# Kernel tuning notes

Hardware: AMD Instinct MI355X
Metric: run time of the kernel (lower is better)

## Reference

```python
import jax, jax.numpy as jnp
import numpy as np

EPS = 1e-5

def _bn(x, gamma, beta):
    # x: [B, N, C]; training-mode BatchNorm1d over (B, N)
    mu = jnp.mean(x, axis=(0, 1))
    var = jnp.var(x, axis=(0, 1))
    return (x - mu) * jax.lax.rsqrt(var + EPS) * gamma + beta


def setup_inputs() -> dict:
    key = jax.random.key(0)
    ks = jax.random.split(key, 32)
    B, N = 16, 8192
    enc_dim, mem_dim = 1024, 1024
    feat_dim = enc_dim + mem_dim  # 2048
    n_points = 2048
    s = 0.02
    d = {
        'partial': jax.random.normal(ks[0], (B, N, 3), jnp.float32),
        # first_conv: Conv1d(3,128,1) + BN(128) + ReLU + Conv1d(128,256,1)
        'W1': jax.random.normal(ks[1], (128, 3), jnp.float32) * s,
        'b1': jnp.zeros((128,), jnp.float32),
        'g1': jnp.ones((128,), jnp.float32),
        'be1': jnp.zeros((128,), jnp.float32),
        'W2': jax.random.normal(ks[2], (256, 128), jnp.float32) * s,
        'b2': jnp.zeros((256,), jnp.float32),
        # second_conv: Conv1d(512,512,1) + BN(512) + ReLU + Conv1d(512,enc_dim,1)
        'W3': jax.random.normal(ks[3], (512, 512), jnp.float32) * s,
        'b3': jnp.zeros((512,), jnp.float32),
        'g2': jnp.ones((512,), jnp.float32),
        'be2': jnp.zeros((512,), jnp.float32),
        'W4': jax.random.normal(ks[4], (enc_dim, 512), jnp.float32) * s,
        'b4': jnp.zeros((enc_dim,), jnp.float32),
        # MemoryModule gates: Linear(enc_dim, mem_dim) x4 + memory param
        'Wf': jax.random.normal(ks[5], (mem_dim, enc_dim), jnp.float32) * s,
        'bf': jnp.zeros((mem_dim,), jnp.float32),
        'Wi': jax.random.normal(ks[6], (mem_dim, enc_dim), jnp.float32) * s,
        'bi': jnp.zeros((mem_dim,), jnp.float32),
        'Wo': jax.random.normal(ks[7], (mem_dim, enc_dim), jnp.float32) * s,
        'bo': jnp.zeros((mem_dim,), jnp.float32),
        'Wc': jax.random.normal(ks[8], (mem_dim, enc_dim), jnp.float32) * s,
        'bc': jnp.zeros((mem_dim,), jnp.float32),
        'mem': jax.random.normal(ks[9], (1, mem_dim), jnp.float32),
        # Decoder MLP: feat_dim->2048->2048->2048->3*n_points
        'D1w': jax.random.normal(ks[10], (2048, feat_dim), jnp.float32) * s,
        'D1b': jnp.zeros((2048,), jnp.float32),
        'D2w': jax.random.normal(ks[11], (2048, 2048), jnp.float32) * s,
        'D2b': jnp.zeros((2048,), jnp.float32),
        'D3w': jax.random.normal(ks[12], (2048, 2048), jnp.float32) * s,
        'D3b': jnp.zeros((2048,), jnp.float32),
        'D4w': jax.random.normal(ks[13], (3 * n_points, 2048), jnp.float32) * s,
        'D4b': jnp.zeros((3 * n_points,), jnp.float32),
    }
    return d


def reference(partial, W1, b1, g1, be1, W2, b2, W3, b3, g2, be2, W4, b4,
              Wf, bf, Wi, bi, Wo, bo, Wc, bc, mem,
              D1w, D1b, D2w, D2b, D3w, D3b, D4w, D4b):
    B, N, _ = partial.shape
    # --- Encoder first_conv (pointwise convs == per-point linear) ---
    f = jnp.einsum('bnc,dc->bnd', partial, W1) + b1          # [B,N,128]
    f = jax.nn.relu(_bn(f, g1, be1))
    f = jnp.einsum('bnc,dc->bnd', f, W2) + b2                # [B,N,256]
    fg = jnp.max(f, axis=1, keepdims=True)                   # [B,1,256]
    f = jnp.concatenate([jnp.broadcast_to(fg, (B, N, 256)), f], axis=-1)  # [B,N,512]
    # --- second_conv ---
    f = jnp.einsum('bnc,dc->bnd', f, W3) + b3                # [B,N,512]
    f = jax.nn.relu(_bn(f, g2, be2))
    f = jnp.einsum('bnc,dc->bnd', f, W4) + b4                # [B,N,enc_dim]
    feat_global = jnp.max(f, axis=1)                         # [B,enc_dim]
    # --- MemoryModule (flag=False: memory not updated) ---
    fgate = jax.nn.sigmoid(feat_global @ Wf.T + bf)
    igate = jax.nn.sigmoid(feat_global @ Wi.T + bi)
    ogate = jax.nn.sigmoid(feat_global @ Wo.T + bo)
    cand = jnp.tanh(feat_global @ Wc.T + bc)
    mem_b = jnp.broadcast_to(mem, fgate.shape)
    h = ogate * jnp.tanh(fgate * mem_b + igate * cand)       # [B,mem_dim]
    feat = jnp.concatenate([feat_global, h], axis=1)         # [B,feat_dim]
    # --- Decoder MLP ---
    z = jax.nn.relu(feat @ D1w.T + D1b)
    z = jax.nn.relu(z @ D2w.T + D2b)
    z = jax.nn.relu(z @ D3w.T + D3b)
    z = z @ D4w.T + D4b                                      # [B, 3*n_points]
    return z.reshape(B, -1, 3)
```

## Files before the change

### kernel.cpp

```cpp
#include <hip/hip_runtime.h>
#include <hip/hip_bf16.h>

typedef __bf16 v8bf __attribute__((ext_vector_type(8)));
typedef float  v4f  __attribute__((ext_vector_type(4)));

#define NPTS (16*8192)
#define RPB  8192

#define GLOAD_LDS16(g, l) __builtin_amdgcn_global_load_lds( \
    (const __attribute__((address_space(1))) void*)(g), \
    (__attribute__((address_space(3))) void*)(l), 16, 0, 0)

__device__ __forceinline__ unsigned fenc(float x){
    unsigned u = __float_as_uint(x);
    return (u & 0x80000000u) ? ~u : (u | 0x80000000u);
}
__device__ __forceinline__ float fdec(unsigned u){
    return __uint_as_float((u & 0x80000000u) ? (u ^ 0x80000000u) : ~u);
}

__device__ __forceinline__ v8bf bn_relu8(v8bf v, float4 s0, float4 s1, float4 h0, float4 h1){
    v8bf r;
    r[0] = (__bf16)fmaxf(fmaf((float)v[0], s0.x, h0.x), 0.f);
    r[1] = (__bf16)fmaxf(fmaf((float)v[1], s0.y, h0.y), 0.f);
    r[2] = (__bf16)fmaxf(fmaf((float)v[2], s0.z, h0.z), 0.f);
    r[3] = (__bf16)fmaxf(fmaf((float)v[3], s0.w, h0.w), 0.f);
    r[4] = (__bf16)fmaxf(fmaf((float)v[4], s1.x, h1.x), 0.f);
    r[5] = (__bf16)fmaxf(fmaf((float)v[5], s1.y, h1.y), 0.f);
    r[6] = (__bf16)fmaxf(fmaf((float)v[6], s1.z, h1.z), 0.f);
    r[7] = (__bf16)fmaxf(fmaf((float)v[7], s1.w, h1.w), 0.f);
    return r;
}

__global__ __launch_bounds__(256) void stats1_k(const float* __restrict__ P,
        const float* __restrict__ W1, const float* __restrict__ b1,
        float* __restrict__ gsum, float* __restrict__ gsumsq)
{
    int tid = threadIdx.x;
    int c = tid & 127, half = tid >> 7;
    float w0 = W1[c*3+0], w1 = W1[c*3+1], w2 = W1[c*3+2], bb = b1[c];
    float s = 0.f, s2 = 0.f;
    int base = blockIdx.x * 512 + half;
    for (int i = 0; i < 256; ++i) {
        int p = base + i*2;
        float x = P[p*3+0], y = P[p*3+1], z = P[p*3+2];
        float v = fmaf(w0,x, fmaf(w1,y, fmaf(w2,z, bb)));
        s += v; s2 = fmaf(v,v,s2);
    }
    __shared__ float ls[256], lq[256];
    ls[tid] = s; lq[tid] = s2;
    __syncthreads();
    if (half == 0) {
        atomicAdd(&gsum[c],   s  + ls[tid+128]);
        atomicAdd(&gsumsq[c], s2 + lq[tid+128]);
    }
}

__global__ void finalize_k(const float* __restrict__ gsum, const float* __restrict__ gsumsq,
        const float* __restrict__ gamma, const float* __restrict__ beta,
        float* __restrict__ scale, float* __restrict__ shift, int C, float invn)
{
    int c = blockIdx.x*blockDim.x + threadIdx.x;
    if (c >= C) return;
    float m   = gsum[c]*invn;
    float var = fmaxf(gsumsq[c]*invn - m*m, 0.f);
    float rs  = rsqrtf(var + 1e-5f);
    float sc  = gamma[c]*rs;
    scale[c] = sc;
    shift[c] = beta[c] - m*sc;
}

__global__ void cvt3_k(const float* __restrict__ W2, const float* __restrict__ W3,
                       const float* __restrict__ W4,
                       __bf16* __restrict__ W2b, __bf16* __restrict__ W3bb,
                       __bf16* __restrict__ W4b)
{
    int i = blockIdx.x*256 + threadIdx.x;
    if (i < 32768) {
        W2b[i] = (__bf16)W2[i];
    } else if (i < 32768 + 131072) {
        int k = i - 32768;
        int r = k >> 8, c = k & 255;
        W3bb[k] = (__bf16)W3[(size_t)r*512 + 256 + c];
    } else if (i < 32768 + 131072 + 524288) {
        int k = i - 163840;
        W4b[k] = (__bf16)W4[k];
    }
}

template<bool STORE, bool DOMAX, bool STATS, int BNMODE, int LOGNB>
__global__ __launch_bounds__(256, 2) void gemm_k(
        const __bf16* __restrict__ A, const __bf16* __restrict__ Bw,
        int K, int Nw,
        const float* __restrict__ bias, int bias_bstride,
        __bf16* __restrict__ Cout, unsigned* __restrict__ maxenc,
        float* __restrict__ gsum, float* __restrict__ gsq,
        const float* __restrict__ scA, const float* __restrict__ shA,
        const float* __restrict__ P3, const float* __restrict__ W1,
        const float* __restrict__ b1)
{
    __shared__ __bf16 As[128*64];
    __shared__ __bf16 Bs[256*64];
    __shared__ float lstat[2][2][256];

    const int tid  = threadIdx.x;
    const int lane = tid & 63;
    const int wave = tid >> 6;
    const int wr = wave >> 1, wc = wave & 1;
    const int nwg   = (int)gridDim.x;
    const int chunk = nwg >> 3;
    const int bi    = (int)blockIdx.x;
    const int li    = (bi & 7) * chunk + (bi >> 3);
    const int m0    = (li >> LOGNB) * 128;
    const int n0    = (li & ((1 << LOGNB) - 1)) * 256;
    const int srow = tid >> 3, sslot = tid & 7;
    const int lrow  = lane >> 3;
    const int swz   = ((lane & 7) ^ lrow) * 8;

    v4f acc[4][8];
    #pragma unroll
    for (int i=0;i<4;i++)
      #pragma unroll
      for (int j=0;j<8;j++) acc[i][j] = (v4f)(0.0f);

    v8bf ra[4];
    auto loadA_pre = [&](int kb){
        int kk = kb + sslot*8;
        float4 s0 = *(const float4*)(scA + kk);
        float4 s1 = *(const float4*)(scA + kk + 4);
        float4 h0 = *(const float4*)(shA + kk);
        float4 h1 = *(const float4*)(shA + kk + 4);
        if constexpr (BNMODE == 1) {
            #pragma unroll
            for (int i=0;i<4;i++){
                int r = i*32 + srow;
                v8bf v = *(const v8bf*)(A + (size_t)(m0+r)*K + kb + sslot*8);
                ra[i] = bn_relu8(v, s0, s1, h0, h1);
            }
        } else if constexpr (BNMODE == 2) {
            float wv0[8], wv1[8], wv2[8], bb[8];
            #pragma unroll
            for (int e=0;e<8;e++){
                wv0[e] = W1[(kk+e)*3+0];
                wv1[e] = W1[(kk+e)*3+1];
                wv2[e] = W1[(kk+e)*3+2];
                bb[e]  = b1[kk+e];
            }
            float sarr[8] = {s0.x,s0.y,s0.z,s0.w,s1.x,s1.y,s1.z,s1.w};
            float harr[8] = {h0.x,h0.y,h0.z,h0.w,h1.x,h1.y,h1.z,h1.w};
            #pragma unroll
            for (int i=0;i<4;i++){
                int r = i*32 + srow;
                const float* pp = P3 + (size_t)(m0+r)*3;
                float x = pp[0], y = pp[1], z = pp[2];
                v8bf v;
                #pragma unroll
                for (int e=0;e<8;e++){
                    float t = fmaf(wv0[e],x, fmaf(wv1[e],y, fmaf(wv2[e],z, bb[e])));
                    t = fmaxf(fmaf(t, sarr[e], harr[e]), 0.f);
                    v[e] = (__bf16)t;
                }
                ra[i] = v;
            }
        }
    };
    auto stageB = [&](int kb){
        #pragma unroll
        for (int j=0;j<8;j++){
            int r0 = (wave*8 + j)*8;
            GLOAD_LDS16(Bw + (size_t)(n0 + r0 + lrow)*K + kb + swz, &Bs[r0*64]);
        }
    };
    auto stageA = [&](int kb){
        #pragma unroll
        for (int j=0;j<4;j++){
            int r0 = (wave*4 + j)*8;
            GLOAD_LDS16(A + (size_t)(m0 + r0 + lrow)*K + kb + swz, &As[r0*64]);
        }
    };

    if constexpr (BNMODE != 0) loadA_pre(0);

    for (int k0 = 0; k0 < K; k0 += 64) {
        __syncthreads();
        stageB(k0);
        if constexpr (BNMODE != 0) {
            #pragma unroll
            for (int i=0;i<4;i++){
                int r = i*32 + srow;
                *(v8bf*)(&As[r*64 + ((sslot ^ (r & 7))<<3)]) = ra[i];
            }
        } else {
            stageA(k0);
        }
        __syncthreads();
        if constexpr (BNMODE != 0) { if (k0 + 64 < K) loadA_pre(k0 + 64); }
        #pragma unroll
        for (int kk = 0; kk < 2; ++kk) {
            v8bf af[4], bfr[8];
            #pragma unroll
            for (int i=0;i<4;i++){
                int arow = wr*64 + i*16 + (lane & 15);
                int sg = kk*4 + (lane >> 4);
                af[i] = *(const v8bf*)(&As[arow*64 + ((sg ^ (arow & 7))<<3)]);
            }
            #pragma unroll
            for (int j=0;j<8;j++){
                int brow = wc*128 + j*16 + (lane & 15);
                int sg = kk*4 + (lane >> 4);
                bfr[j] = *(const v8bf*)(&Bs[brow*64 + ((sg ^ (brow & 7))<<3)]);
            }
            #pragma unroll
            for (int i=0;i<4;i++)
              #pragma unroll
              for (int j=0;j<8;j++)
                acc[i][j] = __builtin_amdgcn_mfma_f32_16x16x32_bf16(af[i], bfr[j], acc[i][j], 0,0,0);
        }
    }

    const int b = m0 / RPB;
    const float* brow_ = bias + (size_t)b * bias_bstride;
    float colmax[8], csum[8], csq[8];
    #pragma unroll
    for (int j=0;j<8;j++){ colmax[j] = -3.402823466e38f; csum[j]=0.f; csq[j]=0.f; }

    #pragma unroll
    for (int i=0;i<4;i++){
        int rbase = m0 + wr*64 + i*16 + ((lane>>4)<<2);
        #pragma unroll
        for (int j=0;j<8;j++){
            int col = n0 + wc*128 + j*16 + (lane & 15);
            float bv = brow_[col];
            #pragma unroll
            for (int q=0;q<4;q++){
                float v = acc[i][j][q] + bv;
                if constexpr (STORE) Cout[(size_t)(rbase+q)*Nw + col] = (__bf16)v;
                if constexpr (DOMAX) colmax[j] = fmaxf(colmax[j], v);
                if constexpr (STATS) { csum[j] += v; csq[j] = fmaf(v,v,csq[j]); }
            }
        }
    }
    if constexpr (DOMAX) {
        #pragma unroll
        for (int j=0;j<8;j++){
            float v = colmax[j];
            v = fmaxf(v, __shfl_xor(v, 16));
            v = fmaxf(v, __shfl_xor(v, 32));
            if (lane < 16) {
                int col = n0 + wc*128 + j*16 + lane;
                atomicMax(&maxenc[(size_t)b*Nw + col], fenc(v));
            }
        }
    }
    if constexpr (STATS) {
        #pragma unroll
        for (int j=0;j<8;j++){
            float s = csum[j], q = csq[j];
            s += __shfl_xor(s, 16); s += __shfl_xor(s, 32);
            q += __shfl_xor(q, 16); q += __shfl_xor(q, 32);
            if (lane < 16) {
                int c = wc*128 + j*16 + lane;
                lstat[0][wr][c] = s;
                lstat[1][wr][c] = q;
            }
        }
        __syncthreads();
        if (tid < 256) {
            float s = lstat[0][0][tid] + lstat[0][1][tid];
            float q = lstat[1][0][tid] + lstat[1][1][tid];
            atomicAdd(&gsum[n0 + tid], s);
            atomicAdd(&gsq [n0 + tid], q);
        }
    }
}

__global__ __launch_bounds__(256) void bias3_k(const unsigned* __restrict__ fge,
        const float* __restrict__ W3, const float* __restrict__ b3,
        float* __restrict__ bias3)
{
    int b = blockIdx.x, tid = threadIdx.x;
    __shared__ float fg[256];
    fg[tid] = fdec(fge[b*256 + tid]);
    __syncthreads();
    for (int d = tid; d < 512; d += 256) {
        const float* wrow = W3 + (size_t)d*512;
        float s = b3[d];
        for (int c = 0; c < 256; c += 4) {
            s = fmaf(fg[c+0], wrow[c+0], s);
            s = fmaf(fg[c+1], wrow[c+1], s);
            s = fmaf(fg[c+2], wrow[c+2], s);
            s = fmaf(fg[c+3], wrow[c+3], s);
        }
        bias3[b*512 + d] = s;
    }
}

__global__ __launch_bounds__(256) void gates2_k(const unsigned* __restrict__ enc,
        const float* __restrict__ Wf, const float* __restrict__ bfv,
        const float* __restrict__ Wi, const float* __restrict__ biv,
        const float* __restrict__ Wo, const float* __restrict__ bov,
        const float* __restrict__ Wc, const float* __restrict__ bcv,
        const float* __restrict__ memv, float* __restrict__ feat)
{
    int tid = threadIdx.x;
    int b = tid & 15;
    int j = blockIdx.x*16 + (tid >> 4);
    const unsigned* xe = enc + (size_t)b*1024;
    const float* rf = Wf + (size_t)j*1024;
    const float* ri = Wi + (size_t)j*1024;
    const float* ro = Wo + (size_t)j*1024;
    const float* rc = Wc + (size_t)j*1024;
    float sf = bfv[j], si = biv[j], so = bov[j], scn = bcv[j];
    for (int c = 0; c < 1024; c += 4) {
        uint4 u = *(const uint4*)(xe + c);
        float4 xv = { fdec(u.x), fdec(u.y), fdec(u.z), fdec(u.w) };
        float4 a  = *(const float4*)(rf + c);
        sf = fmaf(xv.x,a.x, fmaf(xv.y,a.y, fmaf(xv.z,a.z, fmaf(xv.w,a.w, sf))));
        float4 bq = *(const float4*)(ri + c);
        si = fmaf(xv.x,bq.x, fmaf(xv.y,bq.y, fmaf(xv.z,bq.z, fmaf(xv.w,bq.w, si))));
        float4 cq = *(const float4*)(ro + c);
        so = fmaf(xv.x,cq.x, fmaf(xv.y,cq.y, fmaf(xv.z,cq.z, fmaf(xv.w,cq.w, so))));
        float4 dq = *(const float4*)(rc + c);
        scn= fmaf(xv.x,dq.x, fmaf(xv.y,dq.y, fmaf(xv.z,dq.z, fmaf(xv.w,dq.w, scn))));
    }
    float fg = 1.f/(1.f + expf(-sf));
    float ig = 1.f/(1.f + expf(-si));
    float og = 1.f/(1.f + expf(-so));
    float cd = tanhf(scn);
    float h  = og * tanhf(fmaf(fg, memv[j], ig*cd));
    feat[(size_t)b*2048 + j]        = fdec(enc[(size_t)b*1024 + j]);
    feat[(size_t)b*2048 + 1024 + j] = h;
}

template<bool RELU>
__global__ __launch_bounds__(256) void dec2_k(const float* __restrict__ in,
        const float* __restrict__ W, const float* __restrict__ bias,
        float* __restrict__ out, int N)
{
    __shared__ float xin[16*2048];
    int tid = threadIdx.x;
    int lane = tid & 63, wv = tid >> 6;
    #pragma unroll
    for (int j = 0; j < 32; ++j) {
        int blk = wv*32 + j;
        GLOAD_LDS16(in + blk*256 + lane*4, &xin[blk*256]);
    }
    __syncthreads();
    #pragma unroll
    for (int c = 0; c < 2; ++c) {
        int col = blockIdx.x*8 + wv*2 + c;
        const float* wrow = W + (size_t)col*2048;
        float s[16];
        #pragma unroll
        for (int b=0;b<16;b++) s[b]=0.f;
        #pragma unroll
        for (int it = 0; it < 8; ++it) {
            int k = it*256 + lane*4;
            float4 w4 = *(const float4*)(wrow + k);
            #pragma unroll
            for (int b=0;b<16;b++){
                const float* xb = &xin[b*2048 + k];
                s[b] = fmaf(w4.x, xb[0], fmaf(w4.y, xb[1], fmaf(w4.z, xb[2], fmaf(w4.w, xb[3], s[b]))));
            }
        }
        #pragma unroll
        for (int off=32; off; off>>=1){
            #pragma unroll
            for (int b=0;b<16;b++) s[b] += __shfl_xor(s[b], off);
        }
        if (lane == 0) {
            float bv = bias[col];
            #pragma unroll
            for (int b=0;b<16;b++){
                float v = s[b] + bv;
                if (RELU) v = fmaxf(v, 0.f);
                out[(size_t)b*N + col] = v;
            }
        }
    }
}

extern "C" void kernel_launch(void* const* d_in, const int* in_sizes, int n_in,
                              void* d_out, int out_size, void* d_ws, size_t ws_size,
                              hipStream_t stream)
{
    (void)in_sizes; (void)n_in; (void)out_size; (void)ws_size;
    const float* partial = (const float*)d_in[0];
    const float* W1 = (const float*)d_in[1];
    const float* b1 = (const float*)d_in[2];
    const float* g1 = (const float*)d_in[3];
    const float* be1= (const float*)d_in[4];
    const float* W2 = (const float*)d_in[5];
    const float* b2 = (const float*)d_in[6];
    const float* W3 = (const float*)d_in[7];
    const float* b3 = (const float*)d_in[8];
    const float* g2 = (const float*)d_in[9];
    const float* be2= (const float*)d_in[10];
    const float* W4 = (const float*)d_in[11];
    const float* b4 = (const float*)d_in[12];
    const float* Wf = (const float*)d_in[13];
    const float* bfv= (const float*)d_in[14];
    const float* Wi = (const float*)d_in[15];
    const float* biv= (const float*)d_in[16];
    const float* Wo = (const float*)d_in[17];
    const float* bov= (const float*)d_in[18];
    const float* Wc = (const float*)d_in[19];
    const float* bcv= (const float*)d_in[20];
    const float* memv=(const float*)d_in[21];
    const float* D1w= (const float*)d_in[22];
    const float* D1b= (const float*)d_in[23];
    const float* D2w= (const float*)d_in[24];
    const float* D2b= (const float*)d_in[25];
    const float* D3w= (const float*)d_in[26];
    const float* D3b= (const float*)d_in[27];
    const float* D4w= (const float*)d_in[28];
    const float* D4b= (const float*)d_in[29];

    char* w = (char*)d_ws;
    size_t off = 0;
    auto alloc = [&](size_t bytes) -> void* {
        void* p = w + off; off += (bytes + 255) & ~(size_t)255; return p;
    };
    __bf16* f2   = (__bf16*)alloc((size_t)NPTS*256*2);
    __bf16* y3   = (__bf16*)alloc((size_t)NPTS*512*2);
    __bf16* W2b  = (__bf16*)alloc(256*128*2);
    __bf16* W3bb = (__bf16*)alloc(512*256*2);
    __bf16* W4b  = (__bf16*)alloc(1024*512*2);
    char* accbase = (char*)(w + off);
    float* gsum1    = (float*)alloc(128*4);
    float* gsumsq1  = (float*)alloc(128*4);
    float* gsum3    = (float*)alloc(512*4);
    float* gsumsq3  = (float*)alloc(512*4);
    unsigned* fg_enc    = (unsigned*)alloc(16*256*4);
    unsigned* featg_enc = (unsigned*)alloc(16*1024*4);
    size_t accbytes = (size_t)((w + off) - accbase);
    float* scale1 = (float*)alloc(128*4);
    float* shift1 = (float*)alloc(128*4);
    float* scale3 = (float*)alloc(512*4);
    float* shift3 = (float*)alloc(512*4);
    float* bias3  = (float*)alloc(16*512*4);
    float* feat   = (float*)alloc(16*2048*4);
    float* z1     = (float*)alloc(16*2048*4);
    float* z2     = (float*)alloc(16*2048*4);
    float* z3     = (float*)alloc(16*2048*4);

    hipMemsetAsync(accbase, 0, accbytes, stream);

    cvt3_k<<<dim3(2688), 256, 0, stream>>>(W2, W3, W4, W2b, W3bb, W4b);

    stats1_k<<<dim3(256), 256, 0, stream>>>(partial, W1, b1, gsum1, gsumsq1);
    finalize_k<<<dim3(1), 128, 0, stream>>>(gsum1, gsumsq1, g1, be1, scale1, shift1, 128, 1.f/NPTS);

    gemm_k<true,true,false,2,0><<<dim3(1024), 256, 0, stream>>>(
        nullptr, W2b, 128, 256, b2, 0, f2, fg_enc, nullptr, nullptr,
        scale1, shift1, partial, W1, b1);

    bias3_k<<<dim3(16), 256, 0, stream>>>(fg_enc, W3, b3, bias3);

    gemm_k<true,false,true,0,1><<<dim3(2048), 256, 0, stream>>>(
        f2, W3bb, 256, 512, bias3, 512, y3, nullptr, gsum3, gsumsq3,
        nullptr, nullptr, nullptr, nullptr, nullptr);

    finalize_k<<<dim3(2), 256, 0, stream>>>(gsum3, gsumsq3, g2, be2, scale3, shift3, 512, 1.f/NPTS);

    gemm_k<false,true,false,1,2><<<dim3(4096), 256, 0, stream>>>(
        y3, W4b, 512, 1024, b4, 0, nullptr, featg_enc, nullptr, nullptr,
        scale3, shift3, nullptr, nullptr, nullptr);

    gates2_k<<<dim3(64), 256, 0, stream>>>(featg_enc, Wf,bfv, Wi,biv, Wo,bov, Wc,bcv, memv, feat);

    dec2_k<true ><<<dim3(256), 256, 0, stream>>>(feat, D1w, D1b, z1, 2048);
    dec2_k<true ><<<dim3(256), 256, 0, stream>>>(z1,   D2w, D2b, z2, 2048);
    dec2_k<true ><<<dim3(256), 256, 0, stream>>>(z2,   D3w, D3b, z3, 2048);
    dec2_k<false><<<dim3(768), 256, 0, stream>>>(z3,   D4w, D4b, (float*)d_out, 6144);
}
```

Baseline: 481.0 us.

## Compute first BN stats from input moments; process two decoder columns jointly

Replaces the per-channel first-layer BN statistics pass, which evaluated 128 channel outputs for every point, with one pass that accumulates the 9 first and second moments of the 3D input. Each channel's mean and variance are then derived algebraically from W1 and b1, which removes most of the arithmetic and the redundant point reads. Separately, the decoder GEMV kernel now computes both of a wave's output columns in one loop, so each LDS activation read is shared and loaded as float4. The moment-based variance can lose precision through cancellation, and 128 blocks × 4 waves × 9 float atomics all land on the same 9 addresses.

After: 506.9 us. +5.4%, slower.

```diff
diff --git a/kernel.cpp b/kernel.cpp
--- a/kernel.cpp
+++ b/kernel.cpp
@@ -32,28 +32,56 @@
     return r;
 }
 
-__global__ __launch_bounds__(256) void stats1_k(const float* __restrict__ P,
+__global__ __launch_bounds__(256) void mom_k(const float* __restrict__ P,
+        float* __restrict__ mom)
+{
+    int t = blockIdx.x*256 + threadIdx.x;
+    const float* p = P + (size_t)t*12;
+    float4 q0 = *(const float4*)(p);
+    float4 q1 = *(const float4*)(p+4);
+    float4 q2 = *(const float4*)(p+8);
+    float px[4] = {q0.x, q0.w, q1.z, q2.y};
+    float py[4] = {q0.y, q1.x, q1.w, q2.z};
+    float pz[4] = {q0.z, q1.y, q2.x, q2.w};
+    float v[9] = {0,0,0,0,0,0,0,0,0};
+    #pragma unroll
+    for (int i=0;i<4;i++){
+        float x=px[i], y=py[i], z=pz[i];
+        v[0]+=x; v[1]+=y; v[2]+=z;
+        v[3]=fmaf(x,x,v[3]); v[4]=fmaf(x,y,v[4]); v[5]=fmaf(x,z,v[5]);
+        v[6]=fmaf(y,y,v[6]); v[7]=fmaf(y,z,v[7]); v[8]=fmaf(z,z,v[8]);
+    }
+    #pragma unroll
+    for (int off=32; off; off>>=1){
+        #pragma unroll
+        for (int j=0;j<9;j++) v[j] += __shfl_xor(v[j], off);
+    }
+    if ((threadIdx.x & 63) == 0) {
+        #pragma unroll
+        for (int j=0;j<9;j++) atomicAdd(&mom[j], v[j]);
+    }
+}
+
+__global__ void finalize1_k(const float* __restrict__ mom,
         const float* __restrict__ W1, const float* __restrict__ b1,
-        float* __restrict__ gsum, float* __restrict__ gsumsq)
-{
-    int tid = threadIdx.x;
-    int c = tid & 127, half = tid >> 7;
-    float w0 = W1[c*3+0], w1 = W1[c*3+1], w2 = W1[c*3+2], bb = b1[c];
-    float s = 0.f, s2 = 0.f;
-    int base = blockIdx.x * 512 + half;
-    for (int i = 0; i < 256; ++i) {
-        int p = base + i*2;
-        float x = P[p*3+0], y = P[p*3+1], z = P[p*3+2];
-        float v = fmaf(w0,x, fmaf(w1,y, fmaf(w2,z, bb)));
-        s += v; s2 = fmaf(v,v,s2);
-    }
-    __shared__ float ls[256], lq[256];
-    ls[tid] = s; lq[tid] = s2;
-    __syncthreads();
-    if (half == 0) {
-        atomicAdd(&gsum[c],   s  + ls[tid+128]);
-        atomicAdd(&gsumsq[c], s2 + lq[tid+128]);
-    }
+        const float* __restrict__ gamma, const float* __restrict__ beta,
+        float* __restrict__ scale, float* __restrict__ shift)
+{
+    int c = threadIdx.x;
+    float w0=W1[c*3+0], w1=W1[c*3+1], w2=W1[c*3+2], b=b1[c];
+    float S0=mom[0], S1=mom[1], S2=mom[2];
+    float m00=mom[3], m01=mom[4], m02=mom[5], m11=mom[6], m12=mom[7], m22=mom[8];
+    const float invn = 1.f/NPTS;
+    float wS  = fmaf(w0,S0, fmaf(w1,S1, w2*S2));
+    float mean = wS*invn + b;
+    float wMw = w0*w0*m00 + w1*w1*m11 + w2*w2*m22
+              + 2.f*(w0*w1*m01 + w0*w2*m02 + w1*w2*m12);
+    float Ey2 = fmaf(2.f*b, wS, wMw)*invn + b*b;
+    float var = fmaxf(Ey2 - mean*mean, 0.f);
+    float rs  = rsqrtf(var + 1e-5f);
+    float sc  = gamma[c]*rs;
+    scale[c] = sc;
+    shift[c] = beta[c] - mean*sc;
 }
 
 __global__ void finalize_k(const float* __restrict__ gsum, const float* __restrict__ gsumsq,
@@ -346,36 +374,37 @@
         GLOAD_LDS16(in + blk*256 + lane*4, &xin[blk*256]);
     }
     __syncthreads();
-    #pragma unroll
-    for (int c = 0; c < 2; ++c) {
-        int col = blockIdx.x*8 + wv*2 + c;
-        const float* wrow = W + (size_t)col*2048;
-        float s[16];
-        #pragma unroll
-        for (int b=0;b<16;b++) s[b]=0.f;
-        #pragma unroll
-        for (int it = 0; it < 8; ++it) {
-            int k = it*256 + lane*4;
-            float4 w4 = *(const float4*)(wrow + k);
-            #pragma unroll
-            for (int b=0;b<16;b++){
-                const float* xb = &xin[b*2048 + k];
-                s[b] = fmaf(w4.x, xb[0], fmaf(w4.y, xb[1], fmaf(w4.z, xb[2], fmaf(w4.w, xb[3], s[b]))));
-            }
-        }
-        #pragma unroll
-        for (int off=32; off; off>>=1){
-            #pragma unroll
-            for (int b=0;b<16;b++) s[b] += __shfl_xor(s[b], off);
-        }
-        if (lane == 0) {
-            float bv = bias[col];
-            #pragma unroll
-            for (int b=0;b<16;b++){
-                float v = s[b] + bv;
-                if (RELU) v = fmaxf(v, 0.f);
-                out[(size_t)b*N + col] = v;
-            }
+    int col0 = blockIdx.x*8 + wv*2;
+    const float* wrow0 = W + (size_t)col0*2048;
+    const float* wrow1 = W + (size_t)(col0+1)*2048;
+    float s0[16], s1[16];
+    #pragma unroll
+    for (int b=0;b<16;b++){ s0[b]=0.f; s1[b]=0.f; }
+    #pragma unroll
+    for (int it = 0; it < 8; ++it) {
+        int k = it*256 + lane*4;
+        float4 wa = *(const float4*)(wrow0 + k);
+        float4 wb = *(const float4*)(wrow1 + k);
+        #pragma unroll
+        for (int b=0;b<16;b++){
+            float4 xb = *(const float4*)&xin[b*2048 + k];
+            s0[b] = fmaf(wa.x, xb.x, fmaf(wa.y, xb.y, fmaf(wa.z, xb.z, fmaf(wa.w, xb.w, s0[b]))));
+            s1[b] = fmaf(wb.x, xb.x, fmaf(wb.y, xb.y, fmaf(wb.z, xb.z, fmaf(wb.w, xb.w, s1[b]))));
+        }
+    }
+    #pragma unroll
+    for (int off=32; off; off>>=1){
+        #pragma unroll
+        for (int b=0;b<16;b++){ s0[b] += __shfl_xor(s0[b], off); s1[b] += __shfl_xor(s1[b], off); }
+    }
+    if (lane == 0) {
+        float bv0 = bias[col0], bv1 = bias[col0+1];
+        #pragma unroll
+        for (int b=0;b<16;b++){
+            float v0 = s0[b] + bv0, v1 = s1[b] + bv1;
+            if (RELU){ v0 = fmaxf(v0, 0.f); v1 = fmaxf(v1, 0.f); }
+            out[(size_t)b*N + col0]     = v0;
+            out[(size_t)b*N + col0 + 1] = v1;
         }
     }
 }
@@ -427,8 +456,7 @@
     __bf16* W3bb = (__bf16*)alloc(512*256*2);
     __bf16* W4b  = (__bf16*)alloc(1024*512*2);
     char* accbase = (char*)(w + off);
-    float* gsum1    = (float*)alloc(128*4);
-    float* gsumsq1  = (float*)alloc(128*4);
+    float* mom      = (float*)alloc(16*4);
     float* gsum3    = (float*)alloc(512*4);
     float* gsumsq3  = (float*)alloc(512*4);
     unsigned* fg_enc    = (unsigned*)alloc(16*256*4);
@@ -448,8 +476,8 @@
 
     cvt3_k<<<dim3(2688), 256, 0, stream>>>(W2, W3, W4, W2b, W3bb, W4b);
 
-    stats1_k<<<dim3(256), 256, 0, stream>>>(partial, W1, b1, gsum1, gsumsq1);
-    finalize_k<<<dim3(1), 128, 0, stream>>>(gsum1, gsumsq1, g1, be1, scale1, shift1, 128, 1.f/NPTS);
+    mom_k<<<dim3(128), 256, 0, stream>>>(partial, mom);
+    finalize1_k<<<dim3(1), 128, 0, stream>>>(mom, W1, b1, g1, be1, scale1, shift1);
 
     gemm_k<true,true,false,2,0><<<dim3(1024), 256, 0, stream>>>(
         nullptr, W2b, 128, 256, b2, 0, f2, fg_enc, nullptr, nullptr,
```
